# Kernel optimization log

Hardware: AMD Instinct MI355X
Metric: run time of the kernel (lower is better)

The kernel has to match this reference:

```python
import jax, jax.numpy as jnp
import numpy as np

B, C, H, W = 32, 512, 56, 56
GROUPS = 32
CG = C // GROUPS  # channels per group = 16
EPS = 1e-5


def setup_inputs() -> dict:
    key = jax.random.key(0)
    ks = jax.random.split(key, 5)
    return {
        "x": jax.random.normal(ks[0], (B, C, H, W), jnp.float32),
        "w1": jax.random.normal(ks[1], (CG, CG), jnp.float32) * 0.1,   # conv1x1 weight [out,in]
        "b1": jax.random.normal(ks[2], (CG,), jnp.float32) * 0.1,
        "w3": jax.random.normal(ks[3], (CG, CG, 3, 3), jnp.float32) * 0.05,  # conv3x3 OIHW
        "b3": jax.random.normal(ks[4], (CG,), jnp.float32) * 0.1,
        "gn_w": jnp.ones((CG,), jnp.float32),
        "gn_b": jnp.zeros((CG,), jnp.float32),
    }


def reference(x, w1, b1, w3, b3, gn_w, gn_b):
    b, c, h, w = x.shape
    bg = b * GROUPS
    gx = x.reshape(bg, CG, h, w)                                  # group_x
    # directional pooling
    x_h = gx.mean(axis=3, keepdims=True)                          # [bg,cg,h,1]
    x_w = gx.mean(axis=2, keepdims=True).transpose(0, 1, 3, 2)    # [bg,cg,w,1]
    y = jnp.concatenate([x_h, x_w], axis=2)                       # [bg,cg,h+w,1]
    # conv1x1 == channel mixing
    y = jnp.einsum('oc,bcld->bold', w1, y) + b1[None, :, None, None]
    xh = jax.nn.sigmoid(y[:, :, :h])                              # [bg,cg,h,1]
    xw = jax.nn.sigmoid(y[:, :, h:].transpose(0, 1, 3, 2))        # [bg,cg,1,w]
    # GroupNorm(num_groups=cg, num_channels=cg) == per-channel instance norm
    x1 = gx * xh * xw
    mu = x1.mean(axis=(2, 3), keepdims=True)
    var = x1.var(axis=(2, 3), keepdims=True)
    x1 = (x1 - mu) * jax.lax.rsqrt(var + EPS) * gn_w[None, :, None, None] + gn_b[None, :, None, None]
    # conv3x3 branch
    x2 = jax.lax.conv_general_dilated(
        gx, w3, (1, 1), 'SAME',
        dimension_numbers=('NCHW', 'OIHW', 'NCHW')) + b3[None, :, None, None]
    # cross attention weights
    a1 = jax.nn.softmax(x1.mean(axis=(2, 3)), axis=-1)            # [bg,cg]
    a2 = jax.nn.softmax(x2.mean(axis=(2, 3)), axis=-1)            # [bg,cg]
    x1f = x1.reshape(bg, CG, h * w)
    x2f = x2.reshape(bg, CG, h * w)
    out1 = jnp.einsum('bc,bcl->bl', a1, x2f)                      # [bg,hw]
    out2 = jnp.einsum('bc,bcl->bl', a2, x1f)                      # [bg,hw]
    weights = (out1 + out2).reshape(bg, 1, h, w)
    out = gx * jax.nn.sigmoid(weights)
    return out.reshape(b, c, h, w)
```

## Files before the change

### kernel.cpp

```cpp
#include <hip/hip_runtime.h>
#include <math.h>

#define GROUPS 32
#define CG 16
#define HH 56
#define WW 56
#define HW (HH*WW)
#define BG 1024
#define EPS 1e-5f

#define XWS 60
#define XHS 57

#define U_ROW 0
#define U_COL 896
#define U_ST  1792
#define U_X2P 1936
#define U_LS1 2192
#define U_LS2 2208
#define U_SZ  2224

__global__ __launch_bounds__(256, 4) void kF(const float* __restrict__ x,
        const float* __restrict__ w1, const float* __restrict__ b1,
        const float* __restrict__ w3, const float* __restrict__ b3,
        const float* __restrict__ gn_w, const float* __restrict__ gn_b,
        float* __restrict__ out)
{
    const int g = blockIdx.x;
    const int tid = threadIdx.x;
    const float* gx = x + (size_t)g * CG * HW;
    float* og = out + (size_t)g * CG * HW;

    __shared__ float s_u[U_SZ];
    __shared__ float s_xh[CG * XHS];
    __shared__ float s_xw[CG * XWS];
    __shared__ float s_wa[CG * 9 + 1];
    __shared__ float s_asc[CG];
    __shared__ float s_bias;

    if (tid < CG * 9 + 1) {
        float m = gn_b[0];
        #pragma unroll
        for (int c = 1; c < CG; ++c) m = fmaxf(m, gn_b[c]);
        float a1[CG]; float den = 0.f;
        #pragma unroll
        for (int c = 0; c < CG; ++c) { a1[c] = __expf(gn_b[c] - m); den += a1[c]; }
        float inv = 1.f / den;
        if (tid < CG * 9) {
            int ci = tid / 9, k = tid - (tid / 9) * 9;
            float s = 0.f;
            #pragma unroll
            for (int o = 0; o < CG; ++o) s += a1[o] * w3[(size_t)(o * CG + ci) * 9 + k];
            s_wa[tid] = s * inv;
        } else {
            float s = 0.f;
            #pragma unroll
            for (int o = 0; o < CG; ++o) s += a1[o] * b3[o];
            s_wa[CG * 9] = s * inv;
        }
    }

    {
        const int grp = tid >> 4;
        const int q   = tid & 15;
        const float* pc = gx + grp * HW;
        float c0 = 0.f, c1 = 0.f, c2 = 0.f, c3 = 0.f;
        #pragma unroll 2
        for (int row = 0; row < HH; row += 2) {
            float4 va = make_float4(0.f, 0.f, 0.f, 0.f);
            float4 vb = va;
            if (q < 14) {
                va = *(const float4*)(pc + row * WW + q * 4);
                vb = *(const float4*)(pc + (row + 1) * WW + q * 4);
            }
            c0 += va.x + vb.x; c1 += va.y + vb.y;
            c2 += va.z + vb.z; c3 += va.w + vb.w;
            float ra = (va.x + va.y) + (va.z + va.w);
            float rb = (vb.x + vb.y) + (vb.z + vb.w);
            ra += __shfl_down(ra, 8);  rb += __shfl_down(rb, 8);
            ra += __shfl_down(ra, 4);  rb += __shfl_down(rb, 4);
            ra += __shfl_down(ra, 2);  rb += __shfl_down(rb, 2);
            ra += __shfl_down(ra, 1);  rb += __shfl_down(rb, 1);
            if (q == 0) {
                s_u[U_ROW + grp * HH + row]     = ra * (1.0f / WW);
                s_u[U_ROW + grp * HH + row + 1] = rb * (1.0f / WW);
            }
        }
        if (q < 14) {
            s_u[U_COL + grp * WW + q * 4 + 0] = c0 * (1.0f / HH);
            s_u[U_COL + grp * WW + q * 4 + 1] = c1 * (1.0f / HH);
            s_u[U_COL + grp * WW + q * 4 + 2] = c2 * (1.0f / HH);
            s_u[U_COL + grp * WW + q * 4 + 3] = c3 * (1.0f / HH);
        }
    }
    __syncthreads();

    for (int t = tid; t < 2 * CG * HH; t += 256) {
        int hpart = (t < CG * HH);
        int tt = hpart ? t : t - CG * HH;
        int o = tt / HH, i = tt - (tt / HH) * HH;
        float v = b1[o];
        #pragma unroll
        for (int c = 0; c < CG; ++c)
            v += w1[o * CG + c] * (hpart ? s_u[U_ROW + c * HH + i]
                                         : s_u[U_COL + c * WW + i]);
        float sg = 1.f / (1.f + __expf(-v));
        if (hpart) s_xh[o * XHS + i] = sg;
        else       s_xw[o * XWS + i] = sg;
    }

    if (tid < CG) {
        const int c = tid;
        float S = 0.f;
        #pragma unroll
        for (int r = 0; r < HH; ++r) S += s_u[U_ROW + c * HH + r];
        float* st = &s_u[U_ST + c * 9];
        st[0] = S * (float)WW;
        st[1] = (float)WW * s_u[U_ROW + c * HH + HH - 1];
        st[2] = (float)WW * s_u[U_ROW + c * HH];
        st[3] = (float)HH * s_u[U_COL + c * WW + WW - 1];
        st[4] = (float)HH * s_u[U_COL + c * WW];
        const float* p = gx + c * HW;
        st[5] = p[0];
        st[6] = p[WW - 1];
        st[7] = p[(HH - 1) * WW];
        st[8] = p[(HH - 1) * WW + WW - 1];
    }
    __syncthreads();

    {
        const int o = tid >> 4, c = tid & 15;
        const float* wp = w3 + (size_t)(o * CG + c) * 9;
        const float* st = &s_u[U_ST + c * 9];
        float S = st[0];
        float acc = 0.f;
        #pragma unroll
        for (int dy = 0; dy < 3; ++dy) {
            float Rv = (dy == 0) ? st[1] : (dy == 2 ? st[2] : 0.f);
            #pragma unroll
            for (int dx = 0; dx < 3; ++dx) {
                float Cv = (dx == 0) ? st[3] : (dx == 2 ? st[4] : 0.f);
                float T = S - Rv - Cv;
                if (dy != 1 && dx != 1)
                    T += (dy == 0) ? ((dx == 0) ? st[8] : st[7])
                                   : ((dx == 0) ? st[6] : st[5]);
                acc += wp[dy * 3 + dx] * T;
            }
        }
        s_u[U_X2P + c * CG + o] = acc;
    }

    {
        const int c = tid >> 4;
        const int q = tid & 15;
        float s1 = 0.f, s2 = 0.f;
        if (q < 14) {
            const float* pc = gx + c * HW;
            float xw0 = s_xw[c * XWS + q * 4 + 0], xw1 = s_xw[c * XWS + q * 4 + 1];
            float xw2 = s_xw[c * XWS + q * 4 + 2], xw3v = s_xw[c * XWS + q * 4 + 3];
            #pragma unroll 4
            for (int row = 0; row < HH; ++row) {
                float4 v = *(const float4*)(pc + row * WW + q * 4);
                float xh = s_xh[c * XHS + row];
                float t0 = v.x * xh * xw0;
                float t1 = v.y * xh * xw1;
                float t2 = v.z * xh * xw2;
                float t3 = v.w * xh * xw3v;
                s1 += (t0 + t1) + (t2 + t3);
                s2 += (t0 * t0 + t1 * t1) + (t2 * t2 + t3 * t3);
            }
        }
        s1 += __shfl_down(s1, 8);  s2 += __shfl_down(s2, 8);
        s1 += __shfl_down(s1, 4);  s2 += __shfl_down(s2, 4);
        s1 += __shfl_down(s1, 2);  s2 += __shfl_down(s2, 2);
        s1 += __shfl_down(s1, 1);  s2 += __shfl_down(s2, 1);
        if (q == 0) { s_u[U_LS1 + c] = s1; s_u[U_LS2 + c] = s2; }
    }
    __syncthreads();

    if (tid < CG) {
        const int o = tid;
        float x2 = (float)HW * b3[o];
        #pragma unroll
        for (int c = 0; c < CG; ++c) x2 += s_u[U_X2P + c * CG + o];

        float mu  = s_u[U_LS1 + o] * (1.0f / HW);
        float var = s_u[U_LS2 + o] * (1.0f / HW) - mu * mu;
        float sc  = gn_w[o] * rsqrtf(var + EPS);
        float sh  = gn_b[o] - mu * sc;

        float v2 = x2 * (1.0f / HW);
        float m = v2;
        #pragma unroll
        for (int off = 8; off; off >>= 1) m = fmaxf(m, __shfl_xor(m, off));
        float e = __expf(v2 - m);
        float den = e;
        #pragma unroll
        for (int off = 8; off; off >>= 1) den += __shfl_xor(den, off);
        float a2 = e / den;

        s_asc[o] = a2 * sc;
        float part = a2 * sh;
        #pragma unroll
        for (int off = 8; off; off >>= 1) part += __shfl_xor(part, off);
        if (o == 0) s_bias = part + s_wa[CG * 9];
    }
    __syncthreads();

    for (int t = tid; t < CG * HH; t += 256) {
        int c = t / HH, y = t - (t / HH) * HH;
        s_xh[c * XHS + y] *= s_asc[c];
    }
    __syncthreads();

    if (tid < 224) {
        const int cc   = tid & 15;
        const int sp   = tid >> 4;
        const int half = sp / 7;
        const int x0   = (sp - half * 7) * 8;
        const int ybase = half * 28;

        float wreg[9];
        #pragma unroll
        for (int i = 0; i < 9; ++i) wreg[i] = s_wa[cc * 9 + i];
        float xwv[8];
        {
            float4 X0 = *(const float4*)&s_xw[cc * XWS + x0];
            float4 X1 = *(const float4*)&s_xw[cc * XWS + x0 + 4];
            xwv[0] = X0.x; xwv[1] = X0.y; xwv[2] = X0.z; xwv[3] = X0.w;
            xwv[4] = X1.x; xwv[5] = X1.y; xwv[6] = X1.z; xwv[7] = X1.w;
        }
        const float bias = s_bias;
        const float* pc = gx + cc * HW + x0;
        float* oc = og + cc * HW + x0;
        const bool lok = (x0 > 0);
        const bool rok = (x0 < 48);

        float rw1[10], rw2[10], rw3[10], rw4[10];

        #define LOADROW(R, W) do {                                         \
            int r_ = (R);                                                  \
            if (r_ >= 0 && r_ < HH) {                                      \
                const float* bp_ = pc + r_ * WW;                           \
                float4 f1_ = *(const float4*)(bp_);                        \
                float4 f2_ = *(const float4*)(bp_ + 4);                    \
                (W)[0] = lok ? bp_[-1] : 0.f;                              \
                (W)[9] = rok ? bp_[8]  : 0.f;                              \
                (W)[1] = f1_.x; (W)[2] = f1_.y; (W)[3] = f1_.z; (W)[4] = f1_.w; \
                (W)[5] = f2_.x; (W)[6] = f2_.y; (W)[7] = f2_.z; (W)[8] = f2_.w; \
            } else {                                                       \
                _Pragma("unroll")                                          \
                for (int i_ = 0; i_ < 10; ++i_) (W)[i_] = 0.f;             \
            }                                                              \
        } while (0)

        LOADROW(ybase - 1, rw1);
        LOADROW(ybase,     rw2);

        for (int p = 0; p < 14; ++p) {
            const int y0 = ybase + 2 * p;
            LOADROW(y0 + 1, rw3);
            LOADROW(y0 + 2, rw4);
            const float gh0 = s_xh[cc * XHS + y0];
            const float gh1 = s_xh[cc * XHS + y0 + 1];

            float acc0[8], acc1[8];
            #pragma unroll
            for (int j = 0; j < 8; ++j) {
                acc0[j] = wreg[0] * rw1[j] + wreg[1] * rw1[j + 1] + wreg[2] * rw1[j + 2]
                        + wreg[3] * rw2[j] + wreg[4] * rw2[j + 1] + wreg[5] * rw2[j + 2]
                        + wreg[6] * rw3[j] + wreg[7] * rw3[j + 1] + wreg[8] * rw3[j + 2]
                        + gh0 * xwv[j] * rw2[j + 1];
                acc1[j] = wreg[0] * rw2[j] + wreg[1] * rw2[j + 1] + wreg[2] * rw2[j + 2]
                        + wreg[3] * rw3[j] + wreg[4] * rw3[j + 1] + wreg[5] * rw3[j + 2]
                        + wreg[6] * rw4[j] + wreg[7] * rw4[j + 1] + wreg[8] * rw4[j + 2]
                        + gh1 * xwv[j] * rw3[j + 1];
            }

            #pragma unroll
            for (int m = 1; m <= 8; m <<= 1) {
                #pragma unroll
                for (int j = 0; j < 8; ++j) {
                    acc0[j] += __shfl_xor(acc0[j], m);
                    acc1[j] += __shfl_xor(acc1[j], m);
                }
            }

            float o0v[8], o1v[8];
            #pragma unroll
            for (int j = 0; j < 8; ++j) {
                o0v[j] = rw2[j + 1] * (1.f / (1.f + __expf(-(acc0[j] + bias))));
                o1v[j] = rw3[j + 1] * (1.f / (1.f + __expf(-(acc1[j] + bias))));
            }
            float* o0 = oc + y0 * WW;
            float* o1 = o0 + WW;
            *(float4*)(o0)     = make_float4(o0v[0], o0v[1], o0v[2], o0v[3]);
            *(float4*)(o0 + 4) = make_float4(o0v[4], o0v[5], o0v[6], o0v[7]);
            *(float4*)(o1)     = make_float4(o1v[0], o1v[1], o1v[2], o1v[3]);
            *(float4*)(o1 + 4) = make_float4(o1v[4], o1v[5], o1v[6], o1v[7]);

            #pragma unroll
            for (int i = 0; i < 10; ++i) { rw1[i] = rw3[i]; rw2[i] = rw4[i]; }
        }
        #undef LOADROW
    }
}

extern "C" void kernel_launch(void* const* d_in, const int* in_sizes, int n_in,
                              void* d_out, int out_size, void* d_ws, size_t ws_size,
                              hipStream_t stream)
{
    const float* x    = (const float*)d_in[0];
    const float* w1   = (const float*)d_in[1];
    const float* b1   = (const float*)d_in[2];
    const float* w3   = (const float*)d_in[3];
    const float* b3   = (const float*)d_in[4];
    const float* gn_w = (const float*)d_in[5];
    const float* gn_b = (const float*)d_in[6];
    float* out = (float*)d_out;
    (void)d_ws; (void)ws_size;

    kF<<<BG, 256, 0, stream>>>(x, w1, b1, w3, b3, gn_w, gn_b, out);
}
```

Baseline: 491.7 us.

## Double block size to 512 threads and split work across more lanes per stage

Raises the block from 256 to 512 threads and remaps each phase to match. Pooling now gives each channel 32 lanes, with two rows handled at once. The GroupNorm statistics pass walks the channel as a flat float4 stream. The final fused conv/sigmoid pass splits the height into four strips of 14 rows instead of two of 28. The aim is more latency hiding and a shorter serial loop per thread inside each group block. The cost is a tighter register budget under launch_bounds(512,8), more shuffle work, and idle threads in the 256-thread stages.

```diff
diff --git a/kernel.cpp b/kernel.cpp
--- a/kernel.cpp
+++ b/kernel.cpp
@@ -20,7 +20,7 @@
 #define U_LS2 2208
 #define U_SZ  2224
 
-__global__ __launch_bounds__(256, 4) void kF(const float* __restrict__ x,
+__global__ __launch_bounds__(512, 8) void kF(const float* __restrict__ x,
         const float* __restrict__ w1, const float* __restrict__ b1,
         const float* __restrict__ w3, const float* __restrict__ b3,
         const float* __restrict__ gn_w, const float* __restrict__ gn_b,
@@ -61,41 +61,36 @@
     }
 
     {
-        const int grp = tid >> 4;
-        const int q   = tid & 15;
+        const int grp  = tid >> 5;
+        const int lane = tid & 31;
+        const int ql   = lane & 15;
+        const int hi   = lane >> 4;
         const float* pc = gx + grp * HW;
         float c0 = 0.f, c1 = 0.f, c2 = 0.f, c3 = 0.f;
-        #pragma unroll 2
         for (int row = 0; row < HH; row += 2) {
-            float4 va = make_float4(0.f, 0.f, 0.f, 0.f);
-            float4 vb = va;
-            if (q < 14) {
-                va = *(const float4*)(pc + row * WW + q * 4);
-                vb = *(const float4*)(pc + (row + 1) * WW + q * 4);
-            }
-            c0 += va.x + vb.x; c1 += va.y + vb.y;
-            c2 += va.z + vb.z; c3 += va.w + vb.w;
-            float ra = (va.x + va.y) + (va.z + va.w);
-            float rb = (vb.x + vb.y) + (vb.z + vb.w);
-            ra += __shfl_down(ra, 8);  rb += __shfl_down(rb, 8);
-            ra += __shfl_down(ra, 4);  rb += __shfl_down(rb, 4);
-            ra += __shfl_down(ra, 2);  rb += __shfl_down(rb, 2);
-            ra += __shfl_down(ra, 1);  rb += __shfl_down(rb, 1);
-            if (q == 0) {
-                s_u[U_ROW + grp * HH + row]     = ra * (1.0f / WW);
-                s_u[U_ROW + grp * HH + row + 1] = rb * (1.0f / WW);
-            }
-        }
-        if (q < 14) {
-            s_u[U_COL + grp * WW + q * 4 + 0] = c0 * (1.0f / HH);
-            s_u[U_COL + grp * WW + q * 4 + 1] = c1 * (1.0f / HH);
-            s_u[U_COL + grp * WW + q * 4 + 2] = c2 * (1.0f / HH);
-            s_u[U_COL + grp * WW + q * 4 + 3] = c3 * (1.0f / HH);
-        }
-    }
-    __syncthreads();
-
-    for (int t = tid; t < 2 * CG * HH; t += 256) {
+            const int r = row + hi;
+            float4 v = make_float4(0.f, 0.f, 0.f, 0.f);
+            if (ql < 14) v = *(const float4*)(pc + r * WW + ql * 4);
+            c0 += v.x; c1 += v.y; c2 += v.z; c3 += v.w;
+            float rs = (v.x + v.y) + (v.z + v.w);
+            rs += __shfl_xor(rs, 8);
+            rs += __shfl_xor(rs, 4);
+            rs += __shfl_xor(rs, 2);
+            rs += __shfl_xor(rs, 1);
+            if (ql == 0) s_u[U_ROW + grp * HH + r] = rs * (1.0f / WW);
+        }
+        c0 += __shfl_xor(c0, 16); c1 += __shfl_xor(c1, 16);
+        c2 += __shfl_xor(c2, 16); c3 += __shfl_xor(c3, 16);
+        if (hi == 0 && ql < 14) {
+            s_u[U_COL + grp * WW + ql * 4 + 0] = c0 * (1.0f / HH);
+            s_u[U_COL + grp * WW + ql * 4 + 1] = c1 * (1.0f / HH);
+            s_u[U_COL + grp * WW + ql * 4 + 2] = c2 * (1.0f / HH);
+            s_u[U_COL + grp * WW + ql * 4 + 3] = c3 * (1.0f / HH);
+        }
+    }
+    __syncthreads();
+
+    for (int t = tid; t < 2 * CG * HH; t += 512) {
         int hpart = (t < CG * HH);
         int tt = hpart ? t : t - CG * HH;
         int o = tt / HH, i = tt - (tt / HH) * HH;
@@ -128,7 +123,7 @@
     }
     __syncthreads();
 
-    {
+    if (tid < 256) {
         const int o = tid >> 4, c = tid & 15;
         const float* wp = w3 + (size_t)(o * CG + c) * 9;
         const float* st = &s_u[U_ST + c * 9];
@@ -151,30 +146,28 @@
     }
 
     {
-        const int c = tid >> 4;
-        const int q = tid & 15;
+        const int c    = tid >> 5;
+        const int lane = tid & 31;
+        const float* pc = gx + c * HW;
         float s1 = 0.f, s2 = 0.f;
-        if (q < 14) {
-            const float* pc = gx + c * HW;
-            float xw0 = s_xw[c * XWS + q * 4 + 0], xw1 = s_xw[c * XWS + q * 4 + 1];
-            float xw2 = s_xw[c * XWS + q * 4 + 2], xw3v = s_xw[c * XWS + q * 4 + 3];
-            #pragma unroll 4
-            for (int row = 0; row < HH; ++row) {
-                float4 v = *(const float4*)(pc + row * WW + q * 4);
-                float xh = s_xh[c * XHS + row];
-                float t0 = v.x * xh * xw0;
-                float t1 = v.y * xh * xw1;
-                float t2 = v.z * xh * xw2;
-                float t3 = v.w * xh * xw3v;
-                s1 += (t0 + t1) + (t2 + t3);
-                s2 += (t0 * t0 + t1 * t1) + (t2 * t2 + t3 * t3);
-            }
-        }
-        s1 += __shfl_down(s1, 8);  s2 += __shfl_down(s2, 8);
-        s1 += __shfl_down(s1, 4);  s2 += __shfl_down(s2, 4);
-        s1 += __shfl_down(s1, 2);  s2 += __shfl_down(s2, 2);
-        s1 += __shfl_down(s1, 1);  s2 += __shfl_down(s2, 1);
-        if (q == 0) { s_u[U_LS1 + c] = s1; s_u[U_LS2 + c] = s2; }
+        for (int i = lane; i < 784; i += 32) {
+            int row = i / 14;
+            int q   = i - row * 14;
+            float4 v = *(const float4*)(pc + i * 4);
+            float xh = s_xh[c * XHS + row];
+            float t0 = v.x * xh * s_xw[c * XWS + q * 4 + 0];
+            float t1 = v.y * xh * s_xw[c * XWS + q * 4 + 1];
+            float t2 = v.z * xh * s_xw[c * XWS + q * 4 + 2];
+            float t3 = v.w * xh * s_xw[c * XWS + q * 4 + 3];
+            s1 += (t0 + t1) + (t2 + t3);
+            s2 += (t0 * t0 + t1 * t1) + (t2 * t2 + t3 * t3);
+        }
+        s1 += __shfl_xor(s1, 16);  s2 += __shfl_xor(s2, 16);
+        s1 += __shfl_xor(s1, 8);   s2 += __shfl_xor(s2, 8);
+        s1 += __shfl_xor(s1, 4);   s2 += __shfl_xor(s2, 4);
+        s1 += __shfl_xor(s1, 2);   s2 += __shfl_xor(s2, 2);
+        s1 += __shfl_xor(s1, 1);   s2 += __shfl_xor(s2, 1);
+        if (lane == 0) { s_u[U_LS1 + c] = s1; s_u[U_LS2 + c] = s2; }
     }
     __syncthreads();
 
@@ -207,18 +200,18 @@
     }
     __syncthreads();
 
-    for (int t = tid; t < CG * HH; t += 256) {
+    for (int t = tid; t < CG * HH; t += 512) {
         int c = t / HH, y = t - (t / HH) * HH;
         s_xh[c * XHS + y] *= s_asc[c];
     }
     __syncthreads();
 
-    if (tid < 224) {
+    if (tid < 448) {
         const int cc   = tid & 15;
         const int sp   = tid >> 4;
-        const int half = sp / 7;
-        const int x0   = (sp - half * 7) * 8;
-        const int ybase = half * 28;
+        const int quart = sp / 7;
+        const int x0   = (sp - quart * 7) * 8;
+        const int ybase = quart * 14;
 
         float wreg[9];
         #pragma unroll
@@ -257,7 +250,7 @@
         LOADROW(ybase - 1, rw1);
         LOADROW(ybase,     rw2);
 
-        for (int p = 0; p < 14; ++p) {
+        for (int p = 0; p < 7; ++p) {
             const int y0 = ybase + 2 * p;
             LOADROW(y0 + 1, rw3);
             LOADROW(y0 + 2, rw4);
@@ -286,18 +279,28 @@
                 }
             }
 
-            float o0v[8], o1v[8];
-            #pragma unroll
-            for (int j = 0; j < 8; ++j) {
-                o0v[j] = rw2[j + 1] * (1.f / (1.f + __expf(-(acc0[j] + bias))));
-                o1v[j] = rw3[j + 1] * (1.f / (1.f + __expf(-(acc1[j] + bias))));
-            }
             float* o0 = oc + y0 * WW;
             float* o1 = o0 + WW;
-            *(float4*)(o0)     = make_float4(o0v[0], o0v[1], o0v[2], o0v[3]);
-            *(float4*)(o0 + 4) = make_float4(o0v[4], o0v[5], o0v[6], o0v[7]);
-            *(float4*)(o1)     = make_float4(o1v[0], o1v[1], o1v[2], o1v[3]);
-            *(float4*)(o1 + 4) = make_float4(o1v[4], o1v[5], o1v[6], o1v[7]);
+            *(float4*)(o0) = make_float4(
+                rw2[1] * (1.f / (1.f + __expf(-(acc0[0] + bias)))),
+                rw2[2] * (1.f / (1.f + __expf(-(acc0[1] + bias)))),
+                rw2[3] * (1.f / (1.f + __expf(-(acc0[2] + bias)))),
+                rw2[4] * (1.f / (1.f + __expf(-(acc0[3] + bias)))));
+            *(float4*)(o0 + 4) = make_float4(
+                rw2[5] * (1.f / (1.f + __expf(-(acc0[4] + bias)))),
+                rw2[6] * (1.f / (1.f + __expf(-(acc0[5] + bias)))),
+                rw2[7] * (1.f / (1.f + __expf(-(acc0[6] + bias)))),
+                rw2[8] * (1.f / (1.f + __expf(-(acc0[7] + bias)))));
+            *(float4*)(o1) = make_float4(
+                rw3[1] * (1.f / (1.f + __expf(-(acc1[0] + bias)))),
+                rw3[2] * (1.f / (1.f + __expf(-(acc1[1] + bias)))),
+                rw3[3] * (1.f / (1.f + __expf(-(acc1[2] + bias)))),
+                rw3[4] * (1.f / (1.f + __expf(-(acc1[3] + bias)))));
+            *(float4*)(o1 + 4) = make_float4(
+                rw3[5] * (1.f / (1.f + __expf(-(acc1[4] + bias)))),
+                rw3[6] * (1.f / (1.f + __expf(-(acc1[5] + bias)))),
+                rw3[7] * (1.f / (1.f + __expf(-(acc1[6] + bias)))),
+                rw3[8] * (1.f / (1.f + __expf(-(acc1[7] + bias)))));
 
             #pragma unroll
             for (int i = 0; i < 10; ++i) { rw1[i] = rw3[i]; rw2[i] = rw4[i]; }
@@ -320,5 +323,5 @@
     float* out = (float*)d_out;
     (void)d_ws; (void)ws_size;
 
-    kF<<<BG, 256, 0, stream>>>(x, w1, b1, w3, b3, gn_w, gn_b, out);
+    kF<<<BG, 512, 0, stream>>>(x, w1, b1, w3, b3, gn_w, gn_b, out);
 }
```

Measured after the change: 728.3 us. +48.1%, slower.
